# Performance work log

Hardware: AMD Instinct MI355X
Metric: run time of the kernel (lower is better)

The kernel has to match this reference:

```python
import jax, jax.numpy as jnp
import numpy as np


def setup_inputs() -> dict:
    key = jax.random.key(0)
    k1, k2 = jax.random.split(key)
    x = jax.random.normal(k1, (131072, 256), dtype=jnp.float32)
    centroids = jax.random.normal(k2, (2048, 256), dtype=jnp.float32)
    return {"x": x, "centroids": centroids}


def reference(x, centroids):
    """One k-means step: L2 nearest-centroid assignment + scatter-mean update.

    x:         (n, d) sample vectors
    centroids: (K, d) current centroids
    returns:   (K, d) new centroids
    """
    K = centroids.shape[0]
    # Squared L2 distance argmin; ||x||^2 term is constant per row, drop it.
    # scores[n, K] = ||c_k||^2 - 2 * x_n . c_k
    c_sq = jnp.sum(centroids * centroids, axis=-1)          # (K,)
    scores = c_sq[None, :] - 2.0 * jnp.einsum("nd,kd->nk", x, centroids)
    assigns = jnp.argmin(scores, axis=-1)                    # (n,) int
    # Segment mean update; keep old centroid for empty clusters.
    sums = jax.ops.segment_sum(x, assigns, num_segments=K)   # (K, d)
    counts = jax.ops.segment_sum(jnp.ones((x.shape[0],), x.dtype), assigns,
                                 num_segments=K)             # (K,)
    nonempty = counts > 0
    means = sums / jnp.maximum(counts, 1.0)[:, None]
    new_centroids = jnp.where(nonempty[:, None], means, centroids)
    return new_centroids
```

## Files before the change

### kernel.cpp

```cpp
#include <hip/hip_runtime.h>

typedef unsigned short u16;
typedef unsigned int u32;
typedef unsigned long long u64;
typedef __attribute__((ext_vector_type(4)))  int  i32x4;
typedef __attribute__((ext_vector_type(16))) char i8x16;

#define NPTS 131072
#define DIM  256
#define KC   2048

constexpr float S1  = 0.0625f;
constexpr float S2  = S1 / 254.0f;
constexpr float S3  = S2 * S2 / S1;
constexpr float IS1 = 16.0f;
constexpr float IS2 = 4064.0f;
constexpr float IS3 = 1.0f / S3;
constexpr float W_A = S1 * S1;
constexpr float R2  = 1.0f / 254.0f;

__device__ inline void quant3(float v, char& q1, char& q2, char& q3) {
    float a = fminf(fmaxf(rintf(v * IS1), -127.f), 127.f);
    float r1 = fmaf(-a, S1, v);
    float b = rintf(r1 * IS2);
    float r2 = fmaf(-b, S2, r1);
    float c = rintf(r2 * IS3);
    q1 = (char)a; q2 = (char)b; q3 = (char)c;
}

#define GLD16(gsrc, ldst) \
    __builtin_amdgcn_global_load_lds( \
        (const __attribute__((address_space(1))) void*)(gsrc), \
        (__attribute__((address_space(3))) void*)(ldst), 16, 0, 0)

__global__ void cprep_kernel(const float* __restrict__ cen,
                             char* __restrict__ c_q,
                             int* __restrict__ c_sqi,
                             int* __restrict__ hist,
                             float* __restrict__ sums) {
    if (blockIdx.x < 8) hist[blockIdx.x * 256 + threadIdx.x] = 0;
    ((float4*)sums)[blockIdx.x * 256 + threadIdx.x] = (float4){0.f, 0.f, 0.f, 0.f};
    const int lane = threadIdx.x & 63;
    const int wv   = threadIdx.x >> 6;
    const int n    = blockIdx.x * 4 + wv;
    float4 v = ((const float4*)(cen + (size_t)n * DIM))[lane];
    float ss = v.x * v.x + v.y * v.y + v.z * v.z + v.w * v.w;
    float fv[4] = {v.x, v.y, v.z, v.w};
    char q1[4], q2[4], q3[4];
#pragma unroll
    for (int j = 0; j < 4; ++j) quant3(fv[j], q1[j], q2[j], q3[j]);
    const int g16 = n >> 4, c = n & 15;
    const int kc  = lane >> 4;
    const int kq  = (lane >> 2) & 3;
    const size_t base = ((size_t)((g16 * 4 + kc) * 64 + kq * 16 + c)) * 16
                        + (lane & 3) * 4;
    u32 p1 = (u32)(unsigned char)q1[0] | ((u32)(unsigned char)q1[1] << 8) |
             ((u32)(unsigned char)q1[2] << 16) | ((u32)(unsigned char)q1[3] << 24);
    u32 p2 = (u32)(unsigned char)q2[0] | ((u32)(unsigned char)q2[1] << 8) |
             ((u32)(unsigned char)q2[2] << 16) | ((u32)(unsigned char)q2[3] << 24);
    u32 p3 = (u32)(unsigned char)q3[0] | ((u32)(unsigned char)q3[1] << 8) |
             ((u32)(unsigned char)q3[2] << 16) | ((u32)(unsigned char)q3[3] << 24);
    *(u32*)(c_q + base) = p1;
    *(u32*)(c_q + (size_t)KC * DIM + base) = p2;
    *(u32*)(c_q + (size_t)2 * KC * DIM + base) = p3;
#pragma unroll
    for (int off = 32; off > 0; off >>= 1) ss += __shfl_xor(ss, off);
    if (lane == 0) c_sqi[n] = (int)rintf(ss * (0.5f * 254.0f / W_A));
}

__global__ __launch_bounds__(512, 4) void assign_kernel(
    const float* __restrict__ x, const char* __restrict__ c_q,
    const int* __restrict__ c_sqi, int* __restrict__ assigns,
    int* __restrict__ hist) {
    __shared__ char lds_c[3 * 24576 + 8192];

    const int tid  = threadIdx.x;
    const int lane = tid & 63;
    const int wv   = tid >> 6;
    const int p16  = lane & 15;
    const int kq   = lane >> 4;

    const char* cl1 = c_q;
    const char* cl2 = c_q + (size_t)KC * DIM;
    const char* cl3 = c_q + (size_t)2 * KC * DIM;

    GLD16((const char*)c_sqi + tid * 16, lds_c + 73728 + tid * 16);
    GLD16(cl1 + tid * 16,        lds_c + tid * 16);
    GLD16(cl2 + tid * 16,        lds_c + 8192 + tid * 16);
    GLD16(cl3 + tid * 16,        lds_c + 16384 + tid * 16);
    GLD16(cl1 + 8192 + tid * 16, lds_c + 24576 + tid * 16);
    GLD16(cl2 + 8192 + tid * 16, lds_c + 24576 + 8192 + tid * 16);
    GLD16(cl3 + 8192 + tid * 16, lds_c + 24576 + 16384 + tid * 16);

    const int m = blockIdx.x * 128 + wv * 16 + p16;
    const float4* xr = (const float4*)(x + (size_t)m * DIM);
    i8x16 xq1[4], xq2[4], xq3[4];
#pragma unroll
    for (int kc = 0; kc < 4; ++kc) {
        float tmp[16];
#pragma unroll
        for (int j4 = 0; j4 < 4; ++j4) {
            float4 f = xr[kc * 16 + kq * 4 + j4];
            tmp[j4 * 4 + 0] = f.x; tmp[j4 * 4 + 1] = f.y;
            tmp[j4 * 4 + 2] = f.z; tmp[j4 * 4 + 3] = f.w;
        }
        i8x16 v1, v2, v3;
#pragma unroll
        for (int j = 0; j < 16; ++j) {
            char a, b, c;
            quant3(tmp[j], a, b, c);
            v1[j] = a; v2[j] = b; v3[j] = c;
        }
        xq1[kc] = v1; xq2[kc] = v2; xq3[kc] = v3;
    }

    float best = 3.4e38f;
    int bidx = 0;
    int b3 = 0;
    const int* csqL = (const int*)(lds_c + 73728);

    for (int t = 0; t < 64; ++t) {
        if (t == 63) {
            asm volatile("s_waitcnt vmcnt(0)" ::: "memory");
        } else {
            asm volatile("s_waitcnt vmcnt(3)" ::: "memory");
        }
        __builtin_amdgcn_s_barrier();
        __builtin_amdgcn_sched_barrier(0);
        if (t + 2 < 64) {
            int pn = b3 + 2; if (pn >= 3) pn -= 3;
            char* d = lds_c + pn * 24576;
            const size_t so = (size_t)(t + 2) * 8192;
            GLD16(cl1 + so + tid * 16, d + tid * 16);
            GLD16(cl2 + so + tid * 16, d + 8192 + tid * 16);
            GLD16(cl3 + so + tid * 16, d + 16384 + tid * 16);
        }
        const char* cb = lds_c + b3 * 24576;
        i32x4 accA0 = {}, accB0 = {}, accC0 = {};
        i32x4 accA1 = {}, accB1 = {}, accC1 = {};
        __builtin_amdgcn_s_setprio(1);
#pragma unroll
        for (int kc = 0; kc < 4; ++kc) {
            const int off = kc * 1024 + lane * 16;
            i32x4 c1a = __builtin_bit_cast(i32x4, *(const i8x16*)(cb + off));
            i32x4 c2a = __builtin_bit_cast(i32x4, *(const i8x16*)(cb + 8192 + off));
            i32x4 c3a = __builtin_bit_cast(i32x4, *(const i8x16*)(cb + 16384 + off));
            i32x4 c1b = __builtin_bit_cast(i32x4, *(const i8x16*)(cb + 4096 + off));
            i32x4 c2b = __builtin_bit_cast(i32x4, *(const i8x16*)(cb + 12288 + off));
            i32x4 c3b = __builtin_bit_cast(i32x4, *(const i8x16*)(cb + 20480 + off));
            i32x4 x1 = __builtin_bit_cast(i32x4, xq1[kc]);
            i32x4 x2 = __builtin_bit_cast(i32x4, xq2[kc]);
            i32x4 x3 = __builtin_bit_cast(i32x4, xq3[kc]);
            accA0 = __builtin_amdgcn_mfma_i32_16x16x64_i8(c1a, x1, accA0, 0, 0, 0);
            accA1 = __builtin_amdgcn_mfma_i32_16x16x64_i8(c1b, x1, accA1, 0, 0, 0);
            accB0 = __builtin_amdgcn_mfma_i32_16x16x64_i8(c1a, x2, accB0, 0, 0, 0);
            accB1 = __builtin_amdgcn_mfma_i32_16x16x64_i8(c1b, x2, accB1, 0, 0, 0);
            accC0 = __builtin_amdgcn_mfma_i32_16x16x64_i8(c2a, x2, accC0, 0, 0, 0);
            accC1 = __builtin_amdgcn_mfma_i32_16x16x64_i8(c2b, x2, accC1, 0, 0, 0);
            accB0 = __builtin_amdgcn_mfma_i32_16x16x64_i8(c2a, x1, accB0, 0, 0, 0);
            accB1 = __builtin_amdgcn_mfma_i32_16x16x64_i8(c2b, x1, accB1, 0, 0, 0);
            accC0 = __builtin_amdgcn_mfma_i32_16x16x64_i8(c1a, x3, accC0, 0, 0, 0);
            accC1 = __builtin_amdgcn_mfma_i32_16x16x64_i8(c1b, x3, accC1, 0, 0, 0);
            accC0 = __builtin_amdgcn_mfma_i32_16x16x64_i8(c3a, x1, accC0, 0, 0, 0);
            accC1 = __builtin_amdgcn_mfma_i32_16x16x64_i8(c3b, x1, accC1, 0, 0, 0);
        }
        __builtin_amdgcn_s_setprio(0);
        b3 += 1; if (b3 == 3) b3 = 0;

        {
            int4 cs0 = *(const int4*)(csqL + t * 32 + kq * 4);
            int4 cs1 = *(const int4*)(csqL + t * 32 + 16 + kq * 4);
            const int n0 = t * 32 + kq * 4;
            int csa0[4] = {cs0.x, cs0.y, cs0.z, cs0.w};
            int csa1[4] = {cs1.x, cs1.y, cs1.z, cs1.w};
#pragma unroll
            for (int r = 0; r < 4; ++r) {
                int D0 = __mul24(accA0[r], 254) + accB0[r];
                float v0 = fmaf((float)accC0[r], -R2, (float)(csa0[r] - D0));
                if (v0 < best) { best = v0; bidx = n0 + r; }
            }
#pragma unroll
            for (int r = 0; r < 4; ++r) {
                int D1 = __mul24(accA1[r], 254) + accB1[r];
                float v1 = fmaf((float)accC1[r], -R2, (float)(csa1[r] - D1));
                if (v1 < best) { best = v1; bidx = n0 + 16 + r; }
            }
        }
    }

    {
        float oval = __shfl_xor(best, 16);
        int   oidx = __shfl_xor(bidx, 16);
        if (oval < best || (oval == best && oidx < bidx)) { best = oval; bidx = oidx; }
        oval = __shfl_xor(best, 32);
        oidx = __shfl_xor(bidx, 32);
        if (oval < best || (oval == best && oidx < bidx)) { best = oval; bidx = oidx; }
    }
    if (lane < 16) {
        assigns[m] = bidx;
        atomicAdd(&hist[bidx], 1);
    }
}

__global__ void scan_kernel(const int* __restrict__ hist,
                            int* __restrict__ base_,
                            int* __restrict__ cursor) {
    __shared__ int tmp[256];
    const int tid = threadIdx.x;
    int v[8], s = 0;
#pragma unroll
    for (int j = 0; j < 8; ++j) { v[j] = hist[tid * 8 + j]; s += v[j]; }
    tmp[tid] = s;
    __syncthreads();
    for (int off = 1; off < 256; off <<= 1) {
        int t = (tid >= off) ? tmp[tid - off] : 0;
        __syncthreads();
        tmp[tid] += t;
        __syncthreads();
    }
    int ex = tmp[tid] - s;
#pragma unroll
    for (int j = 0; j < 8; ++j) {
        base_[tid * 8 + j] = ex;
        cursor[tid * 8 + j] = ex;
        ex += v[j];
    }
}

__global__ void reorder_kernel(const int* __restrict__ assigns,
                               int* __restrict__ cursor,
                               int* __restrict__ order) {
    const int p = blockIdx.x * 256 + threadIdx.x;
    const int a = assigns[p];
    int pos = atomicAdd(&cursor[a], 1);
    order[pos] = p;
}

__global__ void reduce_kernel(const float* __restrict__ x,
                              const int* __restrict__ order,
                              const int* __restrict__ assigns,
                              float* __restrict__ sums) {
    const int tid = threadIdx.x;
    const int r0 = blockIdx.x * 256;
    float acc = 0.f;
    int cur = assigns[order[r0]];
    for (int r = 0; r < 256; r += 4) {
        int p0 = order[r0 + r + 0], p1 = order[r0 + r + 1];
        int p2 = order[r0 + r + 2], p3 = order[r0 + r + 3];
        float v0 = x[(size_t)p0 * DIM + tid];
        float v1 = x[(size_t)p1 * DIM + tid];
        float v2 = x[(size_t)p2 * DIM + tid];
        float v3 = x[(size_t)p3 * DIM + tid];
        int a0 = assigns[p0], a1 = assigns[p1], a2 = assigns[p2], a3 = assigns[p3];
        if (a0 != cur) { unsafeAtomicAdd(&sums[(size_t)cur * DIM + tid], acc); acc = 0.f; cur = a0; }
        acc += v0;
        if (a1 != cur) { unsafeAtomicAdd(&sums[(size_t)cur * DIM + tid], acc); acc = 0.f; cur = a1; }
        acc += v1;
        if (a2 != cur) { unsafeAtomicAdd(&sums[(size_t)cur * DIM + tid], acc); acc = 0.f; cur = a2; }
        acc += v2;
        if (a3 != cur) { unsafeAtomicAdd(&sums[(size_t)cur * DIM + tid], acc); acc = 0.f; cur = a3; }
        acc += v3;
    }
    unsafeAtomicAdd(&sums[(size_t)cur * DIM + tid], acc);
}

__global__ void finalize_kernel(const float* __restrict__ sums,
                                const int* __restrict__ hist,
                                const float* __restrict__ cen,
                                float* __restrict__ out) {
    const int id = blockIdx.x * 256 + threadIdx.x;
    const int k = id >> 6;
    const int cnt = hist[k];
    float4 s = ((const float4*)sums)[id];
    float4 c = ((const float4*)cen)[id];
    float4 o;
    if (cnt > 0) {
        float r = 1.0f / (float)cnt;
        o.x = s.x * r; o.y = s.y * r; o.z = s.z * r; o.w = s.w * r;
    } else {
        o = c;
    }
    ((float4*)out)[id] = o;
}

extern "C" void kernel_launch(void* const* d_in, const int* in_sizes, int n_in,
                              void* d_out, int out_size, void* d_ws, size_t ws_size,
                              hipStream_t stream) {
    (void)in_sizes; (void)n_in; (void)out_size; (void)ws_size;
    const float* x   = (const float*)d_in[0];
    const float* cen = (const float*)d_in[1];
    float* out = (float*)d_out;

    char* ws = (char*)d_ws;
    size_t off = 0;
    char* c_q = (char*)(ws + off);           off += (size_t)3 * KC * DIM;
    int* c_sqi = (int*)(ws + off);           off += (size_t)KC * 4;
    int* assigns = (int*)(ws + off);         off += (size_t)NPTS * 4;
    int* hist = (int*)(ws + off);            off += (size_t)KC * 4;
    int* base_ = (int*)(ws + off);           off += (size_t)KC * 4;
    int* cursor = (int*)(ws + off);          off += (size_t)KC * 4;
    int* order = (int*)(ws + off);           off += (size_t)NPTS * 4;
    float* sums = (float*)(ws + off);        off += (size_t)KC * DIM * 4;

    cprep_kernel<<<KC / 4, 256, 0, stream>>>(cen, c_q, c_sqi, hist, sums);
    assign_kernel<<<NPTS / 128, 512, 0, stream>>>(x, c_q, c_sqi, assigns, hist);
    scan_kernel<<<1, 256, 0, stream>>>(hist, base_, cursor);
    reorder_kernel<<<NPTS / 256, 256, 0, stream>>>(assigns, cursor, order);
    reduce_kernel<<<NPTS / 256, 256, 0, stream>>>(x, order, assigns, sums);
    finalize_kernel<<<KC * 64 / 256, 256, 0, stream>>>(sums, hist, cen, out);
}
```

Baseline: 571.2 us.

## Assign two 16-point tiles per wave to reuse centroid LDS fragments

Each wave of the assign kernel now handles 32 points as two 16-row tiles, so every centroid fragment read from LDS feeds twice as many MFMAs. The block drops to 256 threads, with each thread issuing two async global-to-LDS loads per matrix instead of one, and the vmcnt wait is raised to match. This halves LDS read traffic per MFMA and the number of waves competing for the shared centroid stream. In exchange it doubles the accumulator and quantized-x register footprint, which can lower occupancy; launch bounds move to (256,2).

```diff
diff --git a/kernel.cpp b/kernel.cpp
--- a/kernel.cpp
+++ b/kernel.cpp
@@ -26,6 +26,25 @@
     float r2 = fmaf(-b, S2, r1);
     float c = rintf(r2 * IS3);
     q1 = (char)a; q2 = (char)b; q3 = (char)c;
+}
+
+__device__ inline void quant_frag(const float4* __restrict__ xr, int kc, int kq,
+                                  i8x16& o1, i8x16& o2, i8x16& o3) {
+    float tmp[16];
+#pragma unroll
+    for (int j4 = 0; j4 < 4; ++j4) {
+        float4 f = xr[kc * 16 + kq * 4 + j4];
+        tmp[j4 * 4 + 0] = f.x; tmp[j4 * 4 + 1] = f.y;
+        tmp[j4 * 4 + 2] = f.z; tmp[j4 * 4 + 3] = f.w;
+    }
+    i8x16 v1, v2, v3;
+#pragma unroll
+    for (int j = 0; j < 16; ++j) {
+        char a, b, c;
+        quant3(tmp[j], a, b, c);
+        v1[j] = a; v2[j] = b; v3[j] = c;
+    }
+    o1 = v1; o2 = v2; o3 = v3;
 }
 
 #define GLD16(gsrc, ldst) \
@@ -68,7 +87,7 @@
     if (lane == 0) c_sqi[n] = (int)rintf(ss * (0.5f * 254.0f / W_A));
 }
 
-__global__ __launch_bounds__(512, 4) void assign_kernel(
+__global__ __launch_bounds__(256, 2) void assign_kernel(
     const float* __restrict__ x, const char* __restrict__ c_q,
     const int* __restrict__ c_sqi, int* __restrict__ assigns,
     int* __restrict__ hist) {
@@ -84,38 +103,33 @@
     const char* cl2 = c_q + (size_t)KC * DIM;
     const char* cl3 = c_q + (size_t)2 * KC * DIM;
 
-    GLD16((const char*)c_sqi + tid * 16, lds_c + 73728 + tid * 16);
-    GLD16(cl1 + tid * 16,        lds_c + tid * 16);
-    GLD16(cl2 + tid * 16,        lds_c + 8192 + tid * 16);
-    GLD16(cl3 + tid * 16,        lds_c + 16384 + tid * 16);
-    GLD16(cl1 + 8192 + tid * 16, lds_c + 24576 + tid * 16);
-    GLD16(cl2 + 8192 + tid * 16, lds_c + 24576 + 8192 + tid * 16);
-    GLD16(cl3 + 8192 + tid * 16, lds_c + 24576 + 16384 + tid * 16);
-
-    const int m = blockIdx.x * 128 + wv * 16 + p16;
-    const float4* xr = (const float4*)(x + (size_t)m * DIM);
-    i8x16 xq1[4], xq2[4], xq3[4];
+    GLD16((const char*)c_sqi + tid * 16,         lds_c + 73728 + tid * 16);
+    GLD16((const char*)c_sqi + (tid + 256) * 16, lds_c + 73728 + (tid + 256) * 16);
+#pragma unroll
+    for (int st = 0; st < 2; ++st) {
+        char* d = lds_c + st * 24576;
+        const size_t so = (size_t)st * 8192;
+        GLD16(cl1 + so + tid * 16,        d + tid * 16);
+        GLD16(cl1 + so + 4096 + tid * 16, d + 4096 + tid * 16);
+        GLD16(cl2 + so + tid * 16,        d + 8192 + tid * 16);
+        GLD16(cl2 + so + 4096 + tid * 16, d + 8192 + 4096 + tid * 16);
+        GLD16(cl3 + so + tid * 16,        d + 16384 + tid * 16);
+        GLD16(cl3 + so + 4096 + tid * 16, d + 16384 + 4096 + tid * 16);
+    }
+
+    const int mA = blockIdx.x * 128 + wv * 32 + p16;
+    const int mB = mA + 16;
+    const float4* xrA = (const float4*)(x + (size_t)mA * DIM);
+    const float4* xrB = (const float4*)(x + (size_t)mB * DIM);
+    i8x16 xa1[4], xa2[4], xa3[4], xb1[4], xb2[4], xb3[4];
 #pragma unroll
     for (int kc = 0; kc < 4; ++kc) {
-        float tmp[16];
-#pragma unroll
-        for (int j4 = 0; j4 < 4; ++j4) {
-            float4 f = xr[kc * 16 + kq * 4 + j4];
-            tmp[j4 * 4 + 0] = f.x; tmp[j4 * 4 + 1] = f.y;
-            tmp[j4 * 4 + 2] = f.z; tmp[j4 * 4 + 3] = f.w;
-        }
-        i8x16 v1, v2, v3;
-#pragma unroll
-        for (int j = 0; j < 16; ++j) {
-            char a, b, c;
-            quant3(tmp[j], a, b, c);
-            v1[j] = a; v2[j] = b; v3[j] = c;
-        }
-        xq1[kc] = v1; xq2[kc] = v2; xq3[kc] = v3;
-    }
-
-    float best = 3.4e38f;
-    int bidx = 0;
+        quant_frag(xrA, kc, kq, xa1[kc], xa2[kc], xa3[kc]);
+        quant_frag(xrB, kc, kq, xb1[kc], xb2[kc], xb3[kc]);
+    }
+
+    float bestA = 3.4e38f, bestB = 3.4e38f;
+    int bixA = 0, bixB = 0;
     int b3 = 0;
     const int* csqL = (const int*)(lds_c + 73728);
 
@@ -123,7 +137,7 @@
         if (t == 63) {
             asm volatile("s_waitcnt vmcnt(0)" ::: "memory");
         } else {
-            asm volatile("s_waitcnt vmcnt(3)" ::: "memory");
+            asm volatile("s_waitcnt vmcnt(6)" ::: "memory");
         }
         __builtin_amdgcn_s_barrier();
         __builtin_amdgcn_sched_barrier(0);
@@ -131,13 +145,18 @@
             int pn = b3 + 2; if (pn >= 3) pn -= 3;
             char* d = lds_c + pn * 24576;
             const size_t so = (size_t)(t + 2) * 8192;
-            GLD16(cl1 + so + tid * 16, d + tid * 16);
-            GLD16(cl2 + so + tid * 16, d + 8192 + tid * 16);
-            GLD16(cl3 + so + tid * 16, d + 16384 + tid * 16);
+            GLD16(cl1 + so + tid * 16,        d + tid * 16);
+            GLD16(cl1 + so + 4096 + tid * 16, d + 4096 + tid * 16);
+            GLD16(cl2 + so + tid * 16,        d + 8192 + tid * 16);
+            GLD16(cl2 + so + 4096 + tid * 16, d + 8192 + 4096 + tid * 16);
+            GLD16(cl3 + so + tid * 16,        d + 16384 + tid * 16);
+            GLD16(cl3 + so + 4096 + tid * 16, d + 16384 + 4096 + tid * 16);
         }
         const char* cb = lds_c + b3 * 24576;
-        i32x4 accA0 = {}, accB0 = {}, accC0 = {};
-        i32x4 accA1 = {}, accB1 = {}, accC1 = {};
+        i32x4 accA0a = {}, accB0a = {}, accC0a = {};
+        i32x4 accA1a = {}, accB1a = {}, accC1a = {};
+        i32x4 accA0b = {}, accB0b = {}, accC0b = {};
+        i32x4 accA1b = {}, accB1b = {}, accC1b = {};
         __builtin_amdgcn_s_setprio(1);
 #pragma unroll
         for (int kc = 0; kc < 4; ++kc) {
@@ -148,21 +167,36 @@
             i32x4 c1b = __builtin_bit_cast(i32x4, *(const i8x16*)(cb + 4096 + off));
             i32x4 c2b = __builtin_bit_cast(i32x4, *(const i8x16*)(cb + 12288 + off));
             i32x4 c3b = __builtin_bit_cast(i32x4, *(const i8x16*)(cb + 20480 + off));
-            i32x4 x1 = __builtin_bit_cast(i32x4, xq1[kc]);
-            i32x4 x2 = __builtin_bit_cast(i32x4, xq2[kc]);
-            i32x4 x3 = __builtin_bit_cast(i32x4, xq3[kc]);
-            accA0 = __builtin_amdgcn_mfma_i32_16x16x64_i8(c1a, x1, accA0, 0, 0, 0);
-            accA1 = __builtin_amdgcn_mfma_i32_16x16x64_i8(c1b, x1, accA1, 0, 0, 0);
-            accB0 = __builtin_amdgcn_mfma_i32_16x16x64_i8(c1a, x2, accB0, 0, 0, 0);
-            accB1 = __builtin_amdgcn_mfma_i32_16x16x64_i8(c1b, x2, accB1, 0, 0, 0);
-            accC0 = __builtin_amdgcn_mfma_i32_16x16x64_i8(c2a, x2, accC0, 0, 0, 0);
-            accC1 = __builtin_amdgcn_mfma_i32_16x16x64_i8(c2b, x2, accC1, 0, 0, 0);
-            accB0 = __builtin_amdgcn_mfma_i32_16x16x64_i8(c2a, x1, accB0, 0, 0, 0);
-            accB1 = __builtin_amdgcn_mfma_i32_16x16x64_i8(c2b, x1, accB1, 0, 0, 0);
-            accC0 = __builtin_amdgcn_mfma_i32_16x16x64_i8(c1a, x3, accC0, 0, 0, 0);
-            accC1 = __builtin_amdgcn_mfma_i32_16x16x64_i8(c1b, x3, accC1, 0, 0, 0);
-            accC0 = __builtin_amdgcn_mfma_i32_16x16x64_i8(c3a, x1, accC0, 0, 0, 0);
-            accC1 = __builtin_amdgcn_mfma_i32_16x16x64_i8(c3b, x1, accC1, 0, 0, 0);
+            i32x4 a1 = __builtin_bit_cast(i32x4, xa1[kc]);
+            i32x4 a2 = __builtin_bit_cast(i32x4, xa2[kc]);
+            i32x4 a3 = __builtin_bit_cast(i32x4, xa3[kc]);
+            i32x4 b1 = __builtin_bit_cast(i32x4, xb1[kc]);
+            i32x4 b2 = __builtin_bit_cast(i32x4, xb2[kc]);
+            i32x4 b3v = __builtin_bit_cast(i32x4, xb3[kc]);
+            accA0a = __builtin_amdgcn_mfma_i32_16x16x64_i8(c1a, a1, accA0a, 0, 0, 0);
+            accA0b = __builtin_amdgcn_mfma_i32_16x16x64_i8(c1a, b1, accA0b, 0, 0, 0);
+            accA1a = __builtin_amdgcn_mfma_i32_16x16x64_i8(c1b, a1, accA1a, 0, 0, 0);
+            accA1b = __builtin_amdgcn_mfma_i32_16x16x64_i8(c1b, b1, accA1b, 0, 0, 0);
+            accB0a = __builtin_amdgcn_mfma_i32_16x16x64_i8(c1a, a2, accB0a, 0, 0, 0);
+            accB0b = __builtin_amdgcn_mfma_i32_16x16x64_i8(c1a, b2, accB0b, 0, 0, 0);
+            accB1a = __builtin_amdgcn_mfma_i32_16x16x64_i8(c1b, a2, accB1a, 0, 0, 0);
+            accB1b = __builtin_amdgcn_mfma_i32_16x16x64_i8(c1b, b2, accB1b, 0, 0, 0);
+            accC0a = __builtin_amdgcn_mfma_i32_16x16x64_i8(c2a, a2, accC0a, 0, 0, 0);
+            accC0b = __builtin_amdgcn_mfma_i32_16x16x64_i8(c2a, b2, accC0b, 0, 0, 0);
+            accC1a = __builtin_amdgcn_mfma_i32_16x16x64_i8(c2b, a2, accC1a, 0, 0, 0);
+            accC1b = __builtin_amdgcn_mfma_i32_16x16x64_i8(c2b, b2, accC1b, 0, 0, 0);
+            accB0a = __builtin_amdgcn_mfma_i32_16x16x64_i8(c2a, a1, accB0a, 0, 0, 0);
+            accB0b = __builtin_amdgcn_mfma_i32_16x16x64_i8(c2a, b1, accB0b, 0, 0, 0);
+            accB1a = __builtin_amdgcn_mfma_i32_16x16x64_i8(c2b, a1, accB1a, 0, 0, 0);
+            accB1b = __builtin_amdgcn_mfma_i32_16x16x64_i8(c2b, b1, accB1b, 0, 0, 0);
+            accC0a = __builtin_amdgcn_mfma_i32_16x16x64_i8(c1a, a3, accC0a, 0, 0, 0);
+            accC0b = __builtin_amdgcn_mfma_i32_16x16x64_i8(c1a, b3v, accC0b, 0, 0, 0);
+            accC1a = __builtin_amdgcn_mfma_i32_16x16x64_i8(c1b, a3, accC1a, 0, 0, 0);
+            accC1b = __builtin_amdgcn_mfma_i32_16x16x64_i8(c1b, b3v, accC1b, 0, 0, 0);
+            accC0a = __builtin_amdgcn_mfma_i32_16x16x64_i8(c3a, a1, accC0a, 0, 0, 0);
+            accC0b = __builtin_amdgcn_mfma_i32_16x16x64_i8(c3a, b1, accC0b, 0, 0, 0);
+            accC1a = __builtin_amdgcn_mfma_i32_16x16x64_i8(c3b, a1, accC1a, 0, 0, 0);
+            accC1b = __builtin_amdgcn_mfma_i32_16x16x64_i8(c3b, b1, accC1b, 0, 0, 0);
         }
         __builtin_amdgcn_s_setprio(0);
         b3 += 1; if (b3 == 3) b3 = 0;
@@ -175,30 +209,42 @@
             int csa1[4] = {cs1.x, cs1.y, cs1.z, cs1.w};
 #pragma unroll
             for (int r = 0; r < 4; ++r) {
-                int D0 = __mul24(accA0[r], 254) + accB0[r];
-                float v0 = fmaf((float)accC0[r], -R2, (float)(csa0[r] - D0));
-                if (v0 < best) { best = v0; bidx = n0 + r; }
+                int D0a = __mul24(accA0a[r], 254) + accB0a[r];
+                float v0a = fmaf((float)accC0a[r], -R2, (float)(csa0[r] - D0a));
+                if (v0a < bestA) { bestA = v0a; bixA = n0 + r; }
+                int D0b = __mul24(accA0b[r], 254) + accB0b[r];
+                float v0b = fmaf((float)accC0b[r], -R2, (float)(csa0[r] - D0b));
+                if (v0b < bestB) { bestB = v0b; bixB = n0 + r; }
             }
 #pragma unroll
             for (int r = 0; r < 4; ++r) {
-                int D1 = __mul24(accA1[r], 254) + accB1[r];
-                float v1 = fmaf((float)accC1[r], -R2, (float)(csa1[r] - D1));
-                if (v1 < best) { best = v1; bidx = n0 + 16 + r; }
+                int D1a = __mul24(accA1a[r], 254) + accB1a[r];
+                float v1a = fmaf((float)accC1a[r], -R2, (float)(csa1[r] - D1a));
+                if (v1a < bestA) { bestA = v1a; bixA = n0 + 16 + r; }
+                int D1b = __mul24(accA1b[r], 254) + accB1b[r];
+                float v1b = fmaf((float)accC1b[r], -R2, (float)(csa1[r] - D1b));
+                if (v1b < bestB) { bestB = v1b; bixB = n0 + 16 + r; }
             }
         }
     }
 
     {
-        float oval = __shfl_xor(best, 16);
-        int   oidx = __shfl_xor(bidx, 16);
-        if (oval < best || (oval == best && oidx < bidx)) { best = oval; bidx = oidx; }
-        oval = __shfl_xor(best, 32);
-        oidx = __shfl_xor(bidx, 32);
-        if (oval < best || (oval == best && oidx < bidx)) { best = oval; bidx = oidx; }
+        float ov; int oi;
+        ov = __shfl_xor(bestA, 16); oi = __shfl_xor(bixA, 16);
+        if (ov < bestA || (ov == bestA && oi < bixA)) { bestA = ov; bixA = oi; }
+        ov = __shfl_xor(bestA, 32); oi = __shfl_xor(bixA, 32);
+        if (ov < bestA || (ov == bestA && oi < bixA)) { bestA = ov; bixA = oi; }
+        ov = __shfl_xor(bestB, 16); oi = __shfl_xor(bixB, 16);
+        if (ov < bestB || (ov == bestB && oi < bixB)) { bestB = ov; bixB = oi; }
+        ov = __shfl_xor(bestB, 32); oi = __shfl_xor(bixB, 32);
+        if (ov < bestB || (ov == bestB && oi < bixB)) { bestB = ov; bixB = oi; }
     }
     if (lane < 16) {
-        assigns[m] = bidx;
-        atomicAdd(&hist[bidx], 1);
+        assigns[mA] = bixA;
+        atomicAdd(&hist[bixA], 1);
+    } else if (lane < 32) {
+        assigns[mB] = bixB;
+        atomicAdd(&hist[bixB], 1);
     }
 }
 
@@ -303,7 +349,7 @@
     float* sums = (float*)(ws + off);        off += (size_t)KC * DIM * 4;
 
     cprep_kernel<<<KC / 4, 256, 0, stream>>>(cen, c_q, c_sqi, hist, sums);
-    assign_kernel<<<NPTS / 128, 512, 0, stream>>>(x, c_q, c_sqi, assigns, hist);
+    assign_kernel<<<NPTS / 128, 256, 0, stream>>>(x, c_q, c_sqi, assigns, hist);
     scan_kernel<<<1, 256, 0, stream>>>(hist, base_, cursor);
     reorder_kernel<<<NPTS / 256, 256, 0, stream>>>(assigns, cursor, order);
     reduce_kernel<<<NPTS / 256, 256, 0, stream>>>(x, order, assigns, sums);
```

Result: slower. 585.9 us (+2.6%).

## Replace scan/reorder/segmented-reduce with direct per-point atomic scatter into sums

Applied to the files above, without the earlier changes.

Removes the scan and reorder kernels along with the sorted segmented reduction. Each wave now reads one point's row as float4 and atomically adds all 256 elements into the assigned centroid's sum row. This cuts two kernel launches and the order-array traffic. In exchange it issues about 33M float atomics, which can contend when many points share a cluster, and the float summation order becomes nondeterministic.

```diff
diff --git a/kernel.cpp b/kernel.cpp
--- a/kernel.cpp
+++ b/kernel.cpp
@@ -202,66 +202,24 @@
     }
 }
 
-__global__ void scan_kernel(const int* __restrict__ hist,
-                            int* __restrict__ base_,
-                            int* __restrict__ cursor) {
-    __shared__ int tmp[256];
-    const int tid = threadIdx.x;
-    int v[8], s = 0;
-#pragma unroll
-    for (int j = 0; j < 8; ++j) { v[j] = hist[tid * 8 + j]; s += v[j]; }
-    tmp[tid] = s;
-    __syncthreads();
-    for (int off = 1; off < 256; off <<= 1) {
-        int t = (tid >= off) ? tmp[tid - off] : 0;
-        __syncthreads();
-        tmp[tid] += t;
-        __syncthreads();
-    }
-    int ex = tmp[tid] - s;
-#pragma unroll
-    for (int j = 0; j < 8; ++j) {
-        base_[tid * 8 + j] = ex;
-        cursor[tid * 8 + j] = ex;
-        ex += v[j];
-    }
-}
-
-__global__ void reorder_kernel(const int* __restrict__ assigns,
-                               int* __restrict__ cursor,
-                               int* __restrict__ order) {
-    const int p = blockIdx.x * 256 + threadIdx.x;
-    const int a = assigns[p];
-    int pos = atomicAdd(&cursor[a], 1);
-    order[pos] = p;
-}
-
 __global__ void reduce_kernel(const float* __restrict__ x,
-                              const int* __restrict__ order,
                               const int* __restrict__ assigns,
                               float* __restrict__ sums) {
     const int tid = threadIdx.x;
-    const int r0 = blockIdx.x * 256;
-    float acc = 0.f;
-    int cur = assigns[order[r0]];
-    for (int r = 0; r < 256; r += 4) {
-        int p0 = order[r0 + r + 0], p1 = order[r0 + r + 1];
-        int p2 = order[r0 + r + 2], p3 = order[r0 + r + 3];
-        float v0 = x[(size_t)p0 * DIM + tid];
-        float v1 = x[(size_t)p1 * DIM + tid];
-        float v2 = x[(size_t)p2 * DIM + tid];
-        float v3 = x[(size_t)p3 * DIM + tid];
-        int a0 = assigns[p0], a1 = assigns[p1], a2 = assigns[p2], a3 = assigns[p3];
-        if (a0 != cur) { unsafeAtomicAdd(&sums[(size_t)cur * DIM + tid], acc); acc = 0.f; cur = a0; }
-        acc += v0;
-        if (a1 != cur) { unsafeAtomicAdd(&sums[(size_t)cur * DIM + tid], acc); acc = 0.f; cur = a1; }
-        acc += v1;
-        if (a2 != cur) { unsafeAtomicAdd(&sums[(size_t)cur * DIM + tid], acc); acc = 0.f; cur = a2; }
-        acc += v2;
-        if (a3 != cur) { unsafeAtomicAdd(&sums[(size_t)cur * DIM + tid], acc); acc = 0.f; cur = a3; }
-        acc += v3;
-    }
-    unsafeAtomicAdd(&sums[(size_t)cur * DIM + tid], acc);
+    const int wv  = tid >> 6;
+    const int l   = tid & 63;
+    const int p0  = blockIdx.x * 128;
+#pragma unroll 4
+    for (int i = 0; i < 32; ++i) {
+        const int p = p0 + i * 4 + wv;
+        const int a = assigns[p];
+        float4 v = ((const float4*)(x + (size_t)p * DIM))[l];
+        float* s = sums + (size_t)a * DIM + l * 4;
+        unsafeAtomicAdd(s + 0, v.x);
+        unsafeAtomicAdd(s + 1, v.y);
+        unsafeAtomicAdd(s + 2, v.z);
+        unsafeAtomicAdd(s + 3, v.w);
+    }
 }
 
 __global__ void finalize_kernel(const float* __restrict__ sums,
@@ -297,15 +255,10 @@
     int* c_sqi = (int*)(ws + off);           off += (size_t)KC * 4;
     int* assigns = (int*)(ws + off);         off += (size_t)NPTS * 4;
     int* hist = (int*)(ws + off);            off += (size_t)KC * 4;
-    int* base_ = (int*)(ws + off);           off += (size_t)KC * 4;
-    int* cursor = (int*)(ws + off);          off += (size_t)KC * 4;
-    int* order = (int*)(ws + off);           off += (size_t)NPTS * 4;
     float* sums = (float*)(ws + off);        off += (size_t)KC * DIM * 4;
 
     cprep_kernel<<<KC / 4, 256, 0, stream>>>(cen, c_q, c_sqi, hist, sums);
     assign_kernel<<<NPTS / 128, 512, 0, stream>>>(x, c_q, c_sqi, assigns, hist);
-    scan_kernel<<<1, 256, 0, stream>>>(hist, base_, cursor);
-    reorder_kernel<<<NPTS / 256, 256, 0, stream>>>(assigns, cursor, order);
-    reduce_kernel<<<NPTS / 256, 256, 0, stream>>>(x, order, assigns, sums);
+    reduce_kernel<<<NPTS / 128, 256, 0, stream>>>(x, assigns, sums);
     finalize_kernel<<<KC * 64 / 256, 256, 0, stream>>>(sums, hist, cen, out);
 }
```

New measurement: 1.290 ms. +125.9%, slower.
